# Kernel tuning notes

Hardware: AMD Instinct MI355X
Metric: run time of the kernel (lower is better)

## Reference

```python
import jax, jax.numpy as jnp
import numpy as np

N = 100000
E = 1600000
ENC_EDGE = 32
ENC_NODE = 64
HIDDEN = 128


def setup_inputs() -> dict:
    key = jax.random.key(0)
    ks = jax.random.split(key, 8)
    x = jax.random.normal(ks[0], (N, ENC_NODE), dtype=jnp.float32)
    edge_index = jax.random.randint(ks[1], (2, E), 0, N, dtype=jnp.int64)
    edge_attr = jax.random.normal(ks[2], (E, ENC_EDGE), dtype=jnp.float32)
    u = jax.random.normal(ks[3], (256, ENC_NODE), dtype=jnp.float32)
    batch = jax.random.randint(ks[4], (N,), 0, 256, dtype=jnp.int64)
    # mlp1: Lin(ENC_EDGE+ENC_NODE -> HIDDEN), xavier_uniform weight, bias=0.01
    in1 = ENC_EDGE + ENC_NODE
    lim1 = float(np.sqrt(6.0 / (in1 + HIDDEN)))
    W1 = jax.random.uniform(ks[5], (in1, HIDDEN), minval=-lim1, maxval=lim1, dtype=jnp.float32)
    b1 = jnp.full((HIDDEN,), 0.01, dtype=jnp.float32)
    # mlp2: Lin(HIDDEN+ENC_NODE -> ENC_NODE)
    in2 = HIDDEN + ENC_NODE
    lim2 = float(np.sqrt(6.0 / (in2 + ENC_NODE)))
    W2 = jax.random.uniform(ks[6], (in2, ENC_NODE), minval=-lim2, maxval=lim2, dtype=jnp.float32)
    b2 = jnp.full((ENC_NODE,), 0.01, dtype=jnp.float32)
    return {"x": x, "edge_index": edge_index, "edge_attr": edge_attr,
            "u": u, "batch": batch, "W1": W1, "b1": b1, "W2": W2, "b2": b2}


def reference(x, edge_index, edge_attr, u, batch, W1, b1, W2, b2):
    row, col = edge_index[0], edge_index[1]
    # gather source node features, concat edge features -> [E, 96]
    msg = jnp.concatenate([x[row], edge_attr], axis=1)
    # mlp1 -> [E, HIDDEN]
    msg = msg @ W1 + b1
    # scatter_add into destination nodes -> [N, HIDDEN]
    agg = jax.ops.segment_sum(msg, col, num_segments=x.shape[0])
    # concat with node features, mlp2 -> [N, ENC_NODE]
    out = jnp.concatenate([x, agg], axis=1)
    return out @ W2 + b2
```

## Files before the change

### kernel.cpp

```cpp
#include <hip/hip_runtime.h>

#define NN 100000
#define NE 1600000
#define NBK 196
#define BNODES 512
#define BCAP 8960
#define OVF_CAP 65536
#define EMASK 0x1FFFFF


__device__ __forceinline__ float mcat_val(const float* __restrict__ W1,
                                          const float* __restrict__ W2,
                                          int r, int j) {
    if (r < 64) return W2[r * 64 + j];
    float acc = 0.f;
    if (r < 128) {
        int i = r - 64;
        for (int h = 0; h < 128; ++h)
            acc = fmaf(W1[i * 128 + h], W2[(64 + h) * 64 + j], acc);
    } else {
        int i = r - 128;
        for (int h = 0; h < 128; ++h)
            acc = fmaf(W1[(64 + i) * 128 + h], W2[(64 + h) * 64 + j], acc);
    }
    return acc;
}

__global__ void precompute_kernel(const float* __restrict__ W1,
                                  const float* __restrict__ b1,
                                  const float* __restrict__ W2,
                                  float* __restrict__ Mcat,
                                  float* __restrict__ vb) {
    int idx = blockIdx.x * blockDim.x + threadIdx.x;
    if (idx < 160 * 64) {
        int kb = idx >> 8, j = (idx >> 2) & 63, w = idx & 3;
        Mcat[idx] = mcat_val(W1, W2, kb * 4 + w, j);
    } else if (idx < 160 * 64 + 64) {
        int j = idx - 160 * 64;
        float acc = 0.f;
        for (int h = 0; h < 128; ++h)
            acc = fmaf(b1[h], W2[(64 + h) * 64 + j], acc);
        vb[j] = acc;
    }
}

__device__ __forceinline__ void spill_rec(int* ovf_cnt, int4* ovf, int b, int2 r) {
    int dst = b * BNODES + (int)((unsigned)r.y >> 21);
    int e = r.y & EMASK;
    int op = atomicAdd(ovf_cnt, 1);
    if (op < OVF_CAP) ovf[op] = make_int4(dst, r.x, e, 0);
}

__global__ __launch_bounds__(1024)
void bin_kernel(const int* __restrict__ ei,
                int* __restrict__ gcur,
                int* __restrict__ ovf_cnt,
                int2* __restrict__ recs,
                int4* __restrict__ ovf) {
    __shared__ int2 ring[NBK][32];
    __shared__ int cur[NBK], flushed[NBK];
    int tid = threadIdx.x;
    if (tid < NBK) { cur[tid] = 0; flushed[tid] = 0; }
    __syncthreads();

    const int per = NE / 256;
    int base = blockIdx.x * per;
    for (int it = 0; it < 7; ++it) {
        int idx = it * 1024 + tid;
        if (idx < per) {
            int e = base + idx;
            int src = ei[e], dst = ei[NE + e];
            int b = dst >> 9;
            int p = atomicAdd(&cur[b], 1);
            ring[b][p & 31] = make_int2(src, ((dst & 511) << 21) | e);
        }
        __syncthreads();
        if (tid < NBK) {
            int f = flushed[tid];
            int g8 = ((cur[tid] - f) >> 3) << 3;
            if (g8 > 0) {
                int gb = atomicAdd(&gcur[tid], g8);
                int2* rb = recs + (size_t)tid * BCAP;
                for (int k = 0; k < g8; k += 2) {
                    int2 r0 = ring[tid][(f + k) & 31];
                    int2 r1 = ring[tid][(f + k + 1) & 31];
                    if (gb + k + 1 < BCAP) {
                        *reinterpret_cast<int4*>(&rb[gb + k]) =
                            make_int4(r0.x, r0.y, r1.x, r1.y);
                    } else {
                        spill_rec(ovf_cnt, ovf, tid, r0);
                        spill_rec(ovf_cnt, ovf, tid, r1);
                    }
                }
                flushed[tid] = f + g8;
            }
        }
        __syncthreads();
    }
    if (tid < NBK) {
        int f = flushed[tid];
        int rem = cur[tid] - f;
        if (rem > 0) {
            int gb = atomicAdd(&gcur[tid], rem);
            int2* rb = recs + (size_t)tid * BCAP;
            for (int k = 0; k < rem; ++k) {
                int2 r = ring[tid][(f + k) & 31];
                if (gb + k < BCAP) rb[gb + k] = r;
                else spill_rec(ovf_cnt, ovf, tid, r);
            }
        }
    }
}

__global__ __launch_bounds__(1024)
void sort_kernel(const int* __restrict__ gcur,
                 const int2* __restrict__ recs,
                 int2* __restrict__ ordered,
                 int* __restrict__ row_start,
                 int* __restrict__ counts) {
    __shared__ int cnt[BNODES], s[BNODES], cur[BNODES];
    int b = blockIdx.x, tid = threadIdx.x;
    int nrec = gcur[b]; if (nrec > BCAP) nrec = BCAP;
    const int2* rb = recs + (size_t)b * BCAP;
    int2* ob = ordered + (size_t)b * BCAP;

    if (tid < BNODES) cnt[tid] = 0;
    __syncthreads();
    for (int i = tid; i < nrec; i += 1024)
        atomicAdd(&cnt[(unsigned)rb[i].y >> 21], 1);
    __syncthreads();
    if (tid < BNODES) s[tid] = cnt[tid];
    __syncthreads();
    for (int off = 1; off < BNODES; off <<= 1) {
        int t = 0;
        if (tid < BNODES && tid >= off) t = s[tid - off];
        __syncthreads();
        if (tid < BNODES) s[tid] += t;
        __syncthreads();
    }
    int obase = b * BCAP;
    if (tid < BNODES) {
        int excl = s[tid] - cnt[tid];
        cur[tid] = excl;
        int n = b * BNODES + tid;
        if (n < NN) { row_start[n] = obase + excl; counts[n] = cnt[tid]; }
    }
    __syncthreads();
    for (int i = tid; i < nrec; i += 1024) {
        int2 r = rb[i];
        int dl = (unsigned)r.y >> 21;
        int pos = atomicAdd(&cur[dl], 1);
        ob[pos] = make_int2(r.x, r.y & EMASK);
    }
}

__global__ __launch_bounds__(1024, 2)
void gather_kernel(const float* __restrict__ x,
                   const float* __restrict__ ea,
                   const float* __restrict__ b2,
                   const float* __restrict__ Mcat,
                   const float* __restrict__ vb,
                   const int* __restrict__ row_start,
                   const int* __restrict__ counts,
                   const int2* __restrict__ pairs,
                   float* __restrict__ out) {
    __shared__ __align__(16) float m4[40 * 256];
    __shared__ __align__(16) float v_lds[16][160];
    __shared__ __align__(8)  int2  p_lds[16][64];
    __shared__ float vb_lds[64], b2_lds[64];

    for (int i = threadIdx.x; i < 10240; i += 1024) m4[i] = Mcat[i];
    if (threadIdx.x < 64) {
        vb_lds[threadIdx.x] = vb[threadIdx.x];
        b2_lds[threadIdx.x] = b2[threadIdx.x];
    }
    __syncthreads();

    int wave = threadIdx.x >> 6;
    int lane = threadIdx.x & 63;
    int elane = lane & 31;
    int nwt = gridDim.x * 16;

    for (int n = blockIdx.x * 16 + wave; n < NN; n += nwt) {
        int dcnt = counts[n];
        int c = row_start[n];
        float xa0 = 0.f, xa1 = 0.f, xa2 = 0.f, xa3 = 0.f;
        float e0a = 0.f, e1a = 0.f;
        int rem = dcnt;
        while (rem > 0) {
            int m = rem < 64 ? rem : 64;
            if (lane < m) p_lds[wave][lane] = pairs[c + lane];
            __threadfence_block();
            const int2* pr = p_lds[wave];
            int i = 0;
            for (; i + 4 <= m; i += 4) {
                int2 q0 = pr[i], q1 = pr[i + 1], q2 = pr[i + 2], q3 = pr[i + 3];
                xa0 += x[(size_t)q0.x * 64 + lane];
                xa1 += x[(size_t)q1.x * 64 + lane];
                xa2 += x[(size_t)q2.x * 64 + lane];
                xa3 += x[(size_t)q3.x * 64 + lane];
                int eA = (lane < 32) ? q0.y : q1.y;
                int eB = (lane < 32) ? q2.y : q3.y;
                e0a += ea[(size_t)eA * 32 + elane];
                e1a += ea[(size_t)eB * 32 + elane];
            }
            for (; i + 2 <= m; i += 2) {
                int2 q0 = pr[i], q1 = pr[i + 1];
                xa0 += x[(size_t)q0.x * 64 + lane];
                xa1 += x[(size_t)q1.x * 64 + lane];
                int eA = (lane < 32) ? q0.y : q1.y;
                e0a += ea[(size_t)eA * 32 + elane];
            }
            if (i < m) {
                int2 q0 = pr[i];
                xa0 += x[(size_t)q0.x * 64 + lane];
                if (lane < 32) e0a += ea[(size_t)q0.y * 32 + elane];
            }
            rem -= m;
            c += m;
        }
        float xacc = (xa0 + xa1) + (xa2 + xa3);
        float eacc = e0a + e1a;
        eacc += __shfl_xor(eacc, 32);

        v_lds[wave][lane] = x[(size_t)n * 64 + lane];
        v_lds[wave][64 + lane] = xacc;
        if (lane < 32) v_lds[wave][128 + elane] = eacc;
        __threadfence_block();

        float acc = b2_lds[lane] + (float)dcnt * vb_lds[lane];
        #pragma unroll
        for (int kb = 0; kb < 40; ++kb) {
            float4 vv = *reinterpret_cast<const float4*>(&v_lds[wave][kb * 4]);
            float4 mm = *reinterpret_cast<const float4*>(&m4[kb * 256 + lane * 4]);
            acc = fmaf(vv.x, mm.x, acc);
            acc = fmaf(vv.y, mm.y, acc);
            acc = fmaf(vv.z, mm.z, acc);
            acc = fmaf(vv.w, mm.w, acc);
        }
        out[(size_t)n * 64 + lane] = acc;
    }
}

__global__ void ovf_kernel(const float* __restrict__ x,
                           const float* __restrict__ ea,
                           const float* __restrict__ Mcat,
                           const float* __restrict__ vb,
                           const int* __restrict__ ovf_cnt,
                           const int4* __restrict__ ovf,
                           float* __restrict__ out) {
    int no = *ovf_cnt;
    if (no > OVF_CAP) no = OVF_CAP;
    int wv = (blockIdx.x * blockDim.x + threadIdx.x) >> 6;
    int lane = threadIdx.x & 63;
    int nw = (gridDim.x * blockDim.x) >> 6;
    for (int o = wv; o < no; o += nw) {
        int4 t = ovf[o];
        float acc = vb[lane];
        #pragma unroll
        for (int kb = 16; kb < 32; ++kb) {
            float4 xv = *reinterpret_cast<const float4*>(&x[(size_t)t.y * 64 + (kb - 16) * 4]);
            float4 mm = *reinterpret_cast<const float4*>(&Mcat[kb * 256 + lane * 4]);
            acc = fmaf(xv.x, mm.x, acc);
            acc = fmaf(xv.y, mm.y, acc);
            acc = fmaf(xv.z, mm.z, acc);
            acc = fmaf(xv.w, mm.w, acc);
        }
        #pragma unroll
        for (int kb = 32; kb < 40; ++kb) {
            float4 av = *reinterpret_cast<const float4*>(&ea[(size_t)t.z * 32 + (kb - 32) * 4]);
            float4 mm = *reinterpret_cast<const float4*>(&Mcat[kb * 256 + lane * 4]);
            acc = fmaf(av.x, mm.x, acc);
            acc = fmaf(av.y, mm.y, acc);
            acc = fmaf(av.z, mm.z, acc);
            acc = fmaf(av.w, mm.w, acc);
        }
        atomicAdd(&out[(size_t)t.x * 64 + lane], acc);
    }
}

extern "C" void kernel_launch(void* const* d_in, const int* in_sizes, int n_in,
                              void* d_out, int out_size, void* d_ws, size_t ws_size,
                              hipStream_t stream) {
    const float* x  = (const float*)d_in[0];
    const int*   ei = (const int*)d_in[1];
    const float* ea = (const float*)d_in[2];
    const float* W1 = (const float*)d_in[5];
    const float* b1 = (const float*)d_in[6];
    const float* W2 = (const float*)d_in[7];
    const float* b2 = (const float*)d_in[8];

    float* ws        = (float*)d_ws;
    float* Mcat      = ws;
    float* vb        = ws + 10240;
    int*   gcur      = (int*)(ws + 10496);
    int*   ovf_cnt   = gcur + 200;
    int2*  recs      = (int2*)(ws + 10752);
    int2*  ordered   = recs + (size_t)NBK * BCAP;
    int*   row_start = (int*)(ordered + (size_t)NBK * BCAP);
    int*   counts    = row_start + NN;
    int4*  ovf       = (int4*)(counts + NN);

    (void)hipMemsetAsync(gcur, 0, 256 * sizeof(int), stream);

    precompute_kernel<<<41, 256, 0, stream>>>(W1, b1, W2, Mcat, vb);
    bin_kernel<<<256, 1024, 0, stream>>>(ei, gcur, ovf_cnt, recs, ovf);
    sort_kernel<<<NBK, 1024, 0, stream>>>(gcur, recs, ordered, row_start, counts);
    gather_kernel<<<512, 1024, 0, stream>>>(x, ea, b2, Mcat, vb, row_start,
                                            counts, ordered, (float*)d_out);
    ovf_kernel<<<16, 256, 0, stream>>>(x, ea, Mcat, vb, ovf_cnt, ovf, (float*)d_out);
}
```

Before: 180.3 us.

## Software-pipeline edge-pair and degree loads across node iterations in gather

```diff
diff --git a/kernel.cpp b/kernel.cpp
--- a/kernel.cpp
+++ b/kernel.cpp
@@ -162,7 +162,7 @@
                    const float* __restrict__ vb,
                    const int* __restrict__ row_start,
                    const int* __restrict__ counts,
-                   const int2* __restrict__ pairs,
+                   const long long* __restrict__ pairs,
                    float* __restrict__ out) {
     __shared__ __align__(16) float m4[40 * 256];
     __shared__ __align__(16) float v_lds[16][160];
@@ -181,49 +181,66 @@
     int elane = lane & 31;
     int nwt = gridDim.x * 16;
 
-    for (int n = blockIdx.x * 16 + wave; n < NN; n += nwt) {
-        int dcnt = counts[n];
-        int c = row_start[n];
+    int n0 = blockIdx.x * 16 + wave;
+    int dc0 = 0, c0 = 0, dc1 = 0, c1 = 0;
+    if (n0 < NN)       { dc0 = counts[n0];       c0 = row_start[n0]; }
+    if (n0 + nwt < NN) { dc1 = counts[n0 + nwt]; c1 = row_start[n0 + nwt]; }
+    long long pk = 0;
+    if (n0 < NN) pk = __builtin_nontemporal_load(&pairs[c0 + lane]);
+
+    for (int n = n0; n < NN; n += nwt) {
+        int dcnt = dc0, c = c0;
+        dc0 = dc1; c0 = c1;
+        int n2 = n + 2 * nwt;
+        if (n2 < NN) { dc1 = counts[n2]; c1 = row_start[n2]; }
+
+        p_lds[wave][lane] = make_int2((int)(pk & 0xFFFFFFFFll), (int)(pk >> 32));
+        float selfx = x[(size_t)n * 64 + lane];
+        __threadfence_block();
+        if (n + nwt < NN) pk = __builtin_nontemporal_load(&pairs[c0 + lane]);
+
+        const int2* pr = p_lds[wave];
+        int m = dcnt < 64 ? dcnt : 64;
         float xa0 = 0.f, xa1 = 0.f, xa2 = 0.f, xa3 = 0.f;
         float e0a = 0.f, e1a = 0.f;
-        int rem = dcnt;
-        while (rem > 0) {
-            int m = rem < 64 ? rem : 64;
-            if (lane < m) p_lds[wave][lane] = pairs[c + lane];
-            __threadfence_block();
-            const int2* pr = p_lds[wave];
-            int i = 0;
-            for (; i + 4 <= m; i += 4) {
-                int2 q0 = pr[i], q1 = pr[i + 1], q2 = pr[i + 2], q3 = pr[i + 3];
-                xa0 += x[(size_t)q0.x * 64 + lane];
-                xa1 += x[(size_t)q1.x * 64 + lane];
-                xa2 += x[(size_t)q2.x * 64 + lane];
-                xa3 += x[(size_t)q3.x * 64 + lane];
-                int eA = (lane < 32) ? q0.y : q1.y;
-                int eB = (lane < 32) ? q2.y : q3.y;
-                e0a += ea[(size_t)eA * 32 + elane];
-                e1a += ea[(size_t)eB * 32 + elane];
-            }
-            for (; i + 2 <= m; i += 2) {
-                int2 q0 = pr[i], q1 = pr[i + 1];
-                xa0 += x[(size_t)q0.x * 64 + lane];
-                xa1 += x[(size_t)q1.x * 64 + lane];
-                int eA = (lane < 32) ? q0.y : q1.y;
-                e0a += ea[(size_t)eA * 32 + elane];
-            }
-            if (i < m) {
-                int2 q0 = pr[i];
-                xa0 += x[(size_t)q0.x * 64 + lane];
-                if (lane < 32) e0a += ea[(size_t)q0.y * 32 + elane];
-            }
-            rem -= m;
-            c += m;
-        }
+        int i = 0;
+        for (; i + 4 <= m; i += 4) {
+            int2 q0 = pr[i], q1 = pr[i + 1], q2 = pr[i + 2], q3 = pr[i + 3];
+            xa0 += x[(size_t)q0.x * 64 + lane];
+            xa1 += x[(size_t)q1.x * 64 + lane];
+            xa2 += x[(size_t)q2.x * 64 + lane];
+            xa3 += x[(size_t)q3.x * 64 + lane];
+            int eA = (lane < 32) ? q0.y : q1.y;
+            int eB = (lane < 32) ? q2.y : q3.y;
+            e0a += __builtin_nontemporal_load(&ea[(size_t)eA * 32 + elane]);
+            e1a += __builtin_nontemporal_load(&ea[(size_t)eB * 32 + elane]);
+        }
+        for (; i + 2 <= m; i += 2) {
+            int2 q0 = pr[i], q1 = pr[i + 1];
+            xa0 += x[(size_t)q0.x * 64 + lane];
+            xa1 += x[(size_t)q1.x * 64 + lane];
+            int eA = (lane < 32) ? q0.y : q1.y;
+            e0a += __builtin_nontemporal_load(&ea[(size_t)eA * 32 + elane]);
+        }
+        if (i < m) {
+            int2 q0 = pr[i];
+            xa0 += x[(size_t)q0.x * 64 + lane];
+            if (lane < 32)
+                e0a += __builtin_nontemporal_load(&ea[(size_t)q0.y * 32 + elane]);
+        }
+        for (int t = 64; t < dcnt; ++t) {
+            long long q = pairs[c + t];
+            int qs = (int)(q & 0xFFFFFFFFll);
+            int qe = (int)(q >> 32);
+            xa0 += x[(size_t)qs * 64 + lane];
+            if (lane < 32) e0a += ea[(size_t)qe * 32 + elane];
+        }
+
         float xacc = (xa0 + xa1) + (xa2 + xa3);
         float eacc = e0a + e1a;
         eacc += __shfl_xor(eacc, 32);
 
-        v_lds[wave][lane] = x[(size_t)n * 64 + lane];
+        v_lds[wave][lane] = selfx;
         v_lds[wave][64 + lane] = xacc;
         if (lane < 32) v_lds[wave][128 + elane] = eacc;
         __threadfence_block();
@@ -307,6 +324,7 @@
     bin_kernel<<<256, 1024, 0, stream>>>(ei, gcur, ovf_cnt, recs, ovf);
     sort_kernel<<<NBK, 1024, 0, stream>>>(gcur, recs, ordered, row_start, counts);
     gather_kernel<<<512, 1024, 0, stream>>>(x, ea, b2, Mcat, vb, row_start,
-                                            counts, ordered, (float*)d_out);
+                                            counts, (const long long*)ordered,
+                                            (float*)d_out);
     ovf_kernel<<<16, 256, 0, stream>>>(x, ea, Mcat, vb, ovf_cnt, ovf, (float*)d_out);
 }
```

New measurement: 180.4 us. No clear change (+0.0%).
